# Performance work log

Hardware: AMD Instinct MI355X
Metric: run time of the kernel (lower is better)

Reference implementation:

```python
import jax, jax.numpy as jnp
import numpy as np


def setup_inputs() -> dict:
    key = jax.random.key(0)
    ks = jax.random.split(key, 5)
    n, raw, d, h = 1024, 128, 128, 256
    s = lambda fan: 1.0 / np.sqrt(fan)
    return {
        "x": jax.random.normal(ks[0], (n, raw), jnp.float32),
        "W_enc": jax.random.normal(ks[1], (raw, d), jnp.float32) * s(raw),
        "b_enc": jnp.zeros((d,), jnp.float32),
        "W1": jax.random.normal(ks[2], (2 * d, h), jnp.float32) * s(2 * d),
        "b1": jnp.zeros((h,), jnp.float32),
        "W2": jax.random.normal(ks[3], (h, 1), jnp.float32) * s(h),
        "b2": jnp.zeros((1,), jnp.float32),
    }


def reference(x, W_enc, b_enc, W1, b1, W2, b2):
    # pathVAE.encode stand-in: linear projection to latent mean
    z = x @ W_enc + b_enc                      # [n, d]
    n, d = z.shape
    # Original builds feat[i, j] = concat(z[j], z[i]) of shape [n*n, 2d],
    # then Linear(2d->h). Split W1 so the quadratic concat is never built:
    # h[i, j] = z[j] @ W1[:d] + z[i] @ W1[d:] + b1
    A = z @ W1[:d]                             # acts on the "a" (j) half
    B = z @ W1[d:]                             # acts on the "b" (i) half
    hmat = A[None, :, :] + B[:, None, :] + b1  # [n, n, h]
    hmat = jax.nn.selu(hmat)
    o = hmat @ W2 + b2                         # [n, n, 1]
    o = jax.nn.hard_sigmoid(o)                 # relu6(x+3)/6, same as torch
    return o.reshape(n, n)
```

## Files before the change

kernel.cpp:

```cpp
#include <hip/hip_runtime.h>
#include <math.h>


#define LOG2E       1.4426950408889634f
#define SELU_AS     1.7580993408473766f
#define S_OVER_L2E  0.7282921587620419f

typedef float v2f __attribute__((ext_vector_type(2)));
typedef _Float16 v2h __attribute__((ext_vector_type(2)));
typedef unsigned int u32;

__global__ __launch_bounds__(256) void prep_kernel(
    const float* __restrict__ x, const float* __restrict__ W_enc,
    const float* __restrict__ b_enc, const float* __restrict__ W1,
    const float* __restrict__ b1, const float* __restrict__ W2,
    const float* __restrict__ b2, u32* __restrict__ PAa,
    u32* __restrict__ PAe, u32* __restrict__ PBb, u32* __restrict__ PBe,
    u32* __restrict__ W2h, float* __restrict__ basep)
{
    __shared__ float zs[512];
    int t = threadIdx.x, b = blockIdx.x;
    if (b < 256) {
        int r0 = b << 2;
        int r = t >> 6;
        int dd = (t & 63) << 1;
        const float* xr = x + (size_t)(r0 + r) * 128;
        v2f z = { b_enc[dd], b_enc[dd + 1] };
#pragma unroll 8
        for (int dl = 0; dl < 128; ++dl) {
            float xv = xr[dl];
            v2f xx = { xv, xv };
            v2f wv = *(const v2f*)(W_enc + (size_t)dl * 128 + dd);
            z = __builtin_elementwise_fma(xx, wv, z);
        }
        zs[r * 128 + dd] = z.x;
        zs[r * 128 + dd + 1] = z.y;
        __syncthreads();

        int c = t;
        float b1c = b1[c];
        float accA0 = 0.f, accA1 = 0.f, accA2 = 0.f, accA3 = 0.f;
        float accB0 = b1c, accB1 = b1c, accB2 = b1c, accB3 = b1c;
        const float* w1a = W1 + c;
        const float* w1b = W1 + 128 * 256 + c;
#pragma unroll 4
        for (int dl = 0; dl < 128; ++dl) {
            float wa = w1a[(size_t)dl * 256];
            float wb = w1b[(size_t)dl * 256];
            float z0 = zs[dl], z1 = zs[128 + dl], z2 = zs[256 + dl], z3 = zs[384 + dl];
            accA0 = fmaf(z0, wa, accA0); accB0 = fmaf(z0, wb, accB0);
            accA1 = fmaf(z1, wa, accA1); accB1 = fmaf(z1, wb, accB1);
            accA2 = fmaf(z2, wa, accA2); accB2 = fmaf(z2, wb, accB2);
            accA3 = fmaf(z3, wa, accA3); accB3 = fmaf(z3, wb, accB3);
        }
        float ar[4] = { accA0 * LOG2E, accA1 * LOG2E, accA2 * LOG2E, accA3 * LOG2E };
        float br[4] = { accB0 * LOG2E, accB1 * LOG2E, accB2 * LOG2E, accB3 * LOG2E };
        u32 pa[4], pe[4], pb[4], pf[4];
        bool odd = (c & 1);
#pragma unroll
        for (int r2 = 0; r2 < 4; ++r2) {
            float er = __builtin_amdgcn_exp2f(ar[r2]);
            float fr = __builtin_amdgcn_exp2f(br[r2]);
            float aN = __shfl_xor(ar[r2], 1);
            float eN = __shfl_xor(er, 1);
            float bN = __shfl_xor(br[r2], 1);
            float fN = __shfl_xor(fr, 1);
            pa[r2] = __builtin_bit_cast(u32, __builtin_amdgcn_cvt_pkrtz(ar[r2], aN));
            pe[r2] = __builtin_bit_cast(u32, __builtin_amdgcn_cvt_pkrtz(er, eN));
            pb[r2] = __builtin_bit_cast(u32, __builtin_amdgcn_cvt_pkrtz(bN, br[r2]));
            pf[r2] = __builtin_bit_cast(u32, __builtin_amdgcn_cvt_pkrtz(fN, fr));
        }
        size_t o = (size_t)(c >> 1) * 1024 + r0;
        if (!odd) {
            *(uint4*)(PAa + o) = make_uint4(pa[0], pa[1], pa[2], pa[3]);
            *(uint4*)(PAe + o) = make_uint4(pe[0], pe[1], pe[2], pe[3]);
        } else {
            *(uint4*)(PBb + o) = make_uint4(pb[0], pb[1], pb[2], pb[3]);
            *(uint4*)(PBe + o) = make_uint4(pf[0], pf[1], pf[2], pf[3]);
        }
    } else {
        if (t < 128) {
            W2h[t] = __builtin_bit_cast(u32,
                __builtin_amdgcn_cvt_pkrtz(W2[2 * t], W2[2 * t + 1]));
        }
        if (t < 64) {
            float s = W2[t] + W2[t + 64] + W2[t + 128] + W2[t + 192];
#pragma unroll
            for (int o = 32; o > 0; o >>= 1) s += __shfl_down(s, o);
            if (t == 0) basep[0] = fmaf(-SELU_AS, s, b2[0]);
        }
    }
}

__global__ __launch_bounds__(256) void pair_kernel(
    const u32* __restrict__ PAa, const u32* __restrict__ PAe,
    const u32* __restrict__ PBb, const u32* __restrict__ PBe,
    const u32* __restrict__ W2h, const float* __restrict__ basep,
    float* __restrict__ out)
{
    __shared__ __align__(16) u32 Aa[64 * 64];
    __shared__ __align__(16) u32 Ae[64 * 64];
    __shared__ __align__(16) u32 Bb[64 * 64];
    __shared__ __align__(16) u32 Be[64 * 64];

    int t = threadIdx.x;
    int bj64 = blockIdx.x << 6, bi64 = blockIdx.y << 6;
    int tjx = t & 15, tiy = t >> 4;
    int tj4 = tjx << 2, ti4 = tiy << 2;

    float acc1[4][4], acc2[4][4];
#pragma unroll
    for (int i = 0; i < 4; ++i)
#pragma unroll
        for (int j = 0; j < 4; ++j) { acc1[i][j] = 0.f; acc2[i][j] = 0.f; }

    const v2h hzero = { (_Float16)0.f, (_Float16)0.f };
    const v2h hone  = { (_Float16)1.f, (_Float16)1.f };

    for (int ch = 0; ch < 2; ++ch) {
        if (ch) __syncthreads();
#pragma unroll
        for (int p = 0; p < 4; ++p) {
            int q = (p << 8) + t;
            int k2l = q >> 4;
            int jq = (q & 15) << 2;
            size_t go = (size_t)((ch << 6) + k2l) * 1024;
            *(uint4*)&Aa[q << 2] = *(const uint4*)(PAa + go + bj64 + jq);
            *(uint4*)&Ae[q << 2] = *(const uint4*)(PAe + go + bj64 + jq);
            *(uint4*)&Bb[q << 2] = *(const uint4*)(PBb + go + bi64 + jq);
            *(uint4*)&Be[q << 2] = *(const uint4*)(PBe + go + bi64 + jq);
        }
        __syncthreads();

        const u32* W2c = W2h + (ch << 6);
#pragma unroll 4
        for (int k2 = 0; k2 < 64; ++k2) {
            v2h w2 = __builtin_bit_cast(v2h, W2c[k2]);
            uint4 qa = *(const uint4*)&Aa[(k2 << 6) + tj4];
            uint4 qe = *(const uint4*)&Ae[(k2 << 6) + tj4];
            uint4 qb = *(const uint4*)&Bb[(k2 << 6) + ti4];
            uint4 qf = *(const uint4*)&Be[(k2 << 6) + ti4];
            v2h a[4] = { __builtin_bit_cast(v2h, qa.x), __builtin_bit_cast(v2h, qa.y),
                         __builtin_bit_cast(v2h, qa.z), __builtin_bit_cast(v2h, qa.w) };
            v2h e[4] = { __builtin_bit_cast(v2h, qe.x), __builtin_bit_cast(v2h, qe.y),
                         __builtin_bit_cast(v2h, qe.z), __builtin_bit_cast(v2h, qe.w) };
            v2h bb[4] = { __builtin_bit_cast(v2h, qb.x), __builtin_bit_cast(v2h, qb.y),
                          __builtin_bit_cast(v2h, qb.z), __builtin_bit_cast(v2h, qb.w) };
            v2h ff[4] = { __builtin_bit_cast(v2h, qf.x), __builtin_bit_cast(v2h, qf.y),
                          __builtin_bit_cast(v2h, qf.z), __builtin_bit_cast(v2h, qf.w) };
#pragma unroll
            for (int i = 0; i < 4; ++i) {
#pragma unroll
                for (int j = 0; j < 4; ++j) {
                    v2h t2 = a[j] + bb[i];
                    v2h p2 = e[j] * ff[i];
                    v2h m2 = __builtin_elementwise_max(t2, hzero);
                    v2h n2 = __builtin_elementwise_min(p2, hone);
                    acc1[i][j] = __builtin_amdgcn_fdot2(m2, w2, acc1[i][j], false);
                    acc2[i][j] = __builtin_amdgcn_fdot2(n2, w2, acc2[i][j], false);
                }
            }
        }
    }

    float base = basep[0];
#pragma unroll
    for (int i = 0; i < 4; ++i) {
        float4 o;
        float v0 = fmaf(S_OVER_L2E, acc1[i][0], fmaf(SELU_AS, acc2[i][0], base));
        float v1 = fmaf(S_OVER_L2E, acc1[i][1], fmaf(SELU_AS, acc2[i][1], base));
        float v2 = fmaf(S_OVER_L2E, acc1[i][2], fmaf(SELU_AS, acc2[i][2], base));
        float v3 = fmaf(S_OVER_L2E, acc1[i][3], fmaf(SELU_AS, acc2[i][3], base));
        o.x = __saturatef(v0 * (1.0f / 6.0f) + 0.5f);
        o.y = __saturatef(v1 * (1.0f / 6.0f) + 0.5f);
        o.z = __saturatef(v2 * (1.0f / 6.0f) + 0.5f);
        o.w = __saturatef(v3 * (1.0f / 6.0f) + 0.5f);
        *(float4*)(out + (size_t)(bi64 + ti4 + i) * 1024 + bj64 + tj4) = o;
    }
}

extern "C" void kernel_launch(void* const* d_in, const int* in_sizes, int n_in,
                              void* d_out, int out_size, void* d_ws, size_t ws_size,
                              hipStream_t stream) {
    const float* x     = (const float*)d_in[0];
    const float* W_enc = (const float*)d_in[1];
    const float* b_enc = (const float*)d_in[2];
    const float* W1    = (const float*)d_in[3];
    const float* b1    = (const float*)d_in[4];
    const float* W2    = (const float*)d_in[5];
    const float* b2    = (const float*)d_in[6];
    float* out = (float*)d_out;

    u32* ws = (u32*)d_ws;
    const int PLANE = 128 * 1024;
    u32* PAa = ws;
    u32* PAe = ws + PLANE;
    u32* PBb = ws + 2 * PLANE;
    u32* PBe = ws + 3 * PLANE;
    u32* W2h = ws + 4 * PLANE;
    float* basep = (float*)(ws + 4 * PLANE + 128);

    prep_kernel<<<257, 256, 0, stream>>>(x, W_enc, b_enc, W1, b1, W2, b2,
                                         PAa, PAe, PBb, PBe, W2h, basep);
    pair_kernel<<<dim3(16, 16), 256, 0, stream>>>(PAa, PAe, PBb, PBe, W2h,
                                                  basep, out);
}
```

Before: 116.5 us.

## Split pair kernel over hidden dimension and reduce partials in combine kernel

```diff
diff --git a/kernel.cpp b/kernel.cpp
--- a/kernel.cpp
+++ b/kernel.cpp
@@ -16,7 +16,7 @@
     const float* __restrict__ b1, const float* __restrict__ W2,
     const float* __restrict__ b2, u32* __restrict__ PAa,
     u32* __restrict__ PAe, u32* __restrict__ PBb, u32* __restrict__ PBe,
-    u32* __restrict__ W2h, float* __restrict__ basep)
+    u32* __restrict__ W2m, u32* __restrict__ W2e, float* __restrict__ basep)
 {
     __shared__ float zs[512];
     int t = threadIdx.x, b = blockIdx.x;
@@ -80,8 +80,11 @@
         }
     } else {
         if (t < 128) {
-            W2h[t] = __builtin_bit_cast(u32,
-                __builtin_amdgcn_cvt_pkrtz(W2[2 * t], W2[2 * t + 1]));
+            float w0 = W2[2 * t], w1 = W2[2 * t + 1];
+            W2m[t] = __builtin_bit_cast(u32,
+                __builtin_amdgcn_cvt_pkrtz(S_OVER_L2E * w0, S_OVER_L2E * w1));
+            W2e[t] = __builtin_bit_cast(u32,
+                __builtin_amdgcn_cvt_pkrtz(SELU_AS * w0, SELU_AS * w1));
         }
         if (t < 64) {
             float s = W2[t] + W2[t + 64] + W2[t + 128] + W2[t + 192];
@@ -92,91 +95,101 @@
     }
 }
 
-__global__ __launch_bounds__(256) void pair_kernel(
+__global__ __launch_bounds__(256, 4) void pair_kernel(
     const u32* __restrict__ PAa, const u32* __restrict__ PAe,
     const u32* __restrict__ PBb, const u32* __restrict__ PBe,
-    const u32* __restrict__ W2h, const float* __restrict__ basep,
+    const u32* __restrict__ W2m, const u32* __restrict__ W2e,
+    float* __restrict__ P)
+{
+    __shared__ __align__(16) u32 Aa[32 * 64];
+    __shared__ __align__(16) u32 Ae[32 * 64];
+    __shared__ __align__(16) u32 Bb[32 * 64];
+    __shared__ __align__(16) u32 Be[32 * 64];
+
+    int t = threadIdx.x;
+    int bj64 = blockIdx.x << 6, bi64 = blockIdx.y << 6;
+    int kc = blockIdx.z;
+    int tj4 = (t & 15) << 2, ti4 = (t >> 4) << 2;
+
+    float acc[4][4];
+#pragma unroll
+    for (int i = 0; i < 4; ++i)
+#pragma unroll
+        for (int j = 0; j < 4; ++j) acc[i][j] = 0.f;
+
+    const v2h hzero = { (_Float16)0.f, (_Float16)0.f };
+    const v2h hone  = { (_Float16)1.f, (_Float16)1.f };
+
+#pragma unroll
+    for (int p = 0; p < 2; ++p) {
+        int q = (p << 8) + t;
+        int k2l = q >> 4;
+        int jq = (q & 15) << 2;
+        size_t go = (size_t)((kc << 5) + k2l) * 1024;
+        *(uint4*)&Aa[q << 2] = *(const uint4*)(PAa + go + bj64 + jq);
+        *(uint4*)&Ae[q << 2] = *(const uint4*)(PAe + go + bj64 + jq);
+        *(uint4*)&Bb[q << 2] = *(const uint4*)(PBb + go + bi64 + jq);
+        *(uint4*)&Be[q << 2] = *(const uint4*)(PBe + go + bi64 + jq);
+    }
+    __syncthreads();
+
+    const u32* Wm = W2m + (kc << 5);
+    const u32* We = W2e + (kc << 5);
+#pragma unroll 4
+    for (int k2 = 0; k2 < 32; ++k2) {
+        v2h w2m = __builtin_bit_cast(v2h, Wm[k2]);
+        v2h w2e = __builtin_bit_cast(v2h, We[k2]);
+        uint4 qa = *(const uint4*)&Aa[(k2 << 6) + tj4];
+        uint4 qe = *(const uint4*)&Ae[(k2 << 6) + tj4];
+        uint4 qb = *(const uint4*)&Bb[(k2 << 6) + ti4];
+        uint4 qf = *(const uint4*)&Be[(k2 << 6) + ti4];
+        v2h a[4] = { __builtin_bit_cast(v2h, qa.x), __builtin_bit_cast(v2h, qa.y),
+                     __builtin_bit_cast(v2h, qa.z), __builtin_bit_cast(v2h, qa.w) };
+        v2h e[4] = { __builtin_bit_cast(v2h, qe.x), __builtin_bit_cast(v2h, qe.y),
+                     __builtin_bit_cast(v2h, qe.z), __builtin_bit_cast(v2h, qe.w) };
+        v2h bb[4] = { __builtin_bit_cast(v2h, qb.x), __builtin_bit_cast(v2h, qb.y),
+                      __builtin_bit_cast(v2h, qb.z), __builtin_bit_cast(v2h, qb.w) };
+        v2h ff[4] = { __builtin_bit_cast(v2h, qf.x), __builtin_bit_cast(v2h, qf.y),
+                      __builtin_bit_cast(v2h, qf.z), __builtin_bit_cast(v2h, qf.w) };
+#pragma unroll
+        for (int i = 0; i < 4; ++i) {
+#pragma unroll
+            for (int j = 0; j < 4; ++j) {
+                v2h t2 = a[j] + bb[i];
+                v2h p2 = e[j] * ff[i];
+                v2h m2 = __builtin_elementwise_max(t2, hzero);
+                v2h n2 = __builtin_elementwise_min(p2, hone);
+                acc[i][j] = __builtin_amdgcn_fdot2(m2, w2m, acc[i][j], false);
+                acc[i][j] = __builtin_amdgcn_fdot2(n2, w2e, acc[i][j], false);
+            }
+        }
+    }
+
+    float* Pc = P + ((size_t)kc << 20);
+#pragma unroll
+    for (int i = 0; i < 4; ++i) {
+        float4 o;
+        o.x = acc[i][0]; o.y = acc[i][1]; o.z = acc[i][2]; o.w = acc[i][3];
+        *(float4*)(Pc + (size_t)(bi64 + ti4 + i) * 1024 + bj64 + tj4) = o;
+    }
+}
+
+__global__ __launch_bounds__(256) void combine_kernel(
+    const float* __restrict__ P, const float* __restrict__ basep,
     float* __restrict__ out)
 {
-    __shared__ __align__(16) u32 Aa[64 * 64];
-    __shared__ __align__(16) u32 Ae[64 * 64];
-    __shared__ __align__(16) u32 Bb[64 * 64];
-    __shared__ __align__(16) u32 Be[64 * 64];
-
-    int t = threadIdx.x;
-    int bj64 = blockIdx.x << 6, bi64 = blockIdx.y << 6;
-    int tjx = t & 15, tiy = t >> 4;
-    int tj4 = tjx << 2, ti4 = tiy << 2;
-
-    float acc1[4][4], acc2[4][4];
-#pragma unroll
-    for (int i = 0; i < 4; ++i)
-#pragma unroll
-        for (int j = 0; j < 4; ++j) { acc1[i][j] = 0.f; acc2[i][j] = 0.f; }
-
-    const v2h hzero = { (_Float16)0.f, (_Float16)0.f };
-    const v2h hone  = { (_Float16)1.f, (_Float16)1.f };
-
-    for (int ch = 0; ch < 2; ++ch) {
-        if (ch) __syncthreads();
-#pragma unroll
-        for (int p = 0; p < 4; ++p) {
-            int q = (p << 8) + t;
-            int k2l = q >> 4;
-            int jq = (q & 15) << 2;
-            size_t go = (size_t)((ch << 6) + k2l) * 1024;
-            *(uint4*)&Aa[q << 2] = *(const uint4*)(PAa + go + bj64 + jq);
-            *(uint4*)&Ae[q << 2] = *(const uint4*)(PAe + go + bj64 + jq);
-            *(uint4*)&Bb[q << 2] = *(const uint4*)(PBb + go + bi64 + jq);
-            *(uint4*)&Be[q << 2] = *(const uint4*)(PBe + go + bi64 + jq);
-        }
-        __syncthreads();
-
-        const u32* W2c = W2h + (ch << 6);
-#pragma unroll 4
-        for (int k2 = 0; k2 < 64; ++k2) {
-            v2h w2 = __builtin_bit_cast(v2h, W2c[k2]);
-            uint4 qa = *(const uint4*)&Aa[(k2 << 6) + tj4];
-            uint4 qe = *(const uint4*)&Ae[(k2 << 6) + tj4];
-            uint4 qb = *(const uint4*)&Bb[(k2 << 6) + ti4];
-            uint4 qf = *(const uint4*)&Be[(k2 << 6) + ti4];
-            v2h a[4] = { __builtin_bit_cast(v2h, qa.x), __builtin_bit_cast(v2h, qa.y),
-                         __builtin_bit_cast(v2h, qa.z), __builtin_bit_cast(v2h, qa.w) };
-            v2h e[4] = { __builtin_bit_cast(v2h, qe.x), __builtin_bit_cast(v2h, qe.y),
-                         __builtin_bit_cast(v2h, qe.z), __builtin_bit_cast(v2h, qe.w) };
-            v2h bb[4] = { __builtin_bit_cast(v2h, qb.x), __builtin_bit_cast(v2h, qb.y),
-                          __builtin_bit_cast(v2h, qb.z), __builtin_bit_cast(v2h, qb.w) };
-            v2h ff[4] = { __builtin_bit_cast(v2h, qf.x), __builtin_bit_cast(v2h, qf.y),
-                          __builtin_bit_cast(v2h, qf.z), __builtin_bit_cast(v2h, qf.w) };
-#pragma unroll
-            for (int i = 0; i < 4; ++i) {
-#pragma unroll
-                for (int j = 0; j < 4; ++j) {
-                    v2h t2 = a[j] + bb[i];
-                    v2h p2 = e[j] * ff[i];
-                    v2h m2 = __builtin_elementwise_max(t2, hzero);
-                    v2h n2 = __builtin_elementwise_min(p2, hone);
-                    acc1[i][j] = __builtin_amdgcn_fdot2(m2, w2, acc1[i][j], false);
-                    acc2[i][j] = __builtin_amdgcn_fdot2(n2, w2, acc2[i][j], false);
-                }
-            }
-        }
-    }
-
+    int idx = (blockIdx.x * 256 + threadIdx.x) << 2;
+    float4 p0 = *(const float4*)(P + idx);
+    float4 p1 = *(const float4*)(P + (1 << 20) + idx);
+    float4 p2 = *(const float4*)(P + (2 << 20) + idx);
+    float4 p3 = *(const float4*)(P + (3 << 20) + idx);
     float base = basep[0];
-#pragma unroll
-    for (int i = 0; i < 4; ++i) {
-        float4 o;
-        float v0 = fmaf(S_OVER_L2E, acc1[i][0], fmaf(SELU_AS, acc2[i][0], base));
-        float v1 = fmaf(S_OVER_L2E, acc1[i][1], fmaf(SELU_AS, acc2[i][1], base));
-        float v2 = fmaf(S_OVER_L2E, acc1[i][2], fmaf(SELU_AS, acc2[i][2], base));
-        float v3 = fmaf(S_OVER_L2E, acc1[i][3], fmaf(SELU_AS, acc2[i][3], base));
-        o.x = __saturatef(v0 * (1.0f / 6.0f) + 0.5f);
-        o.y = __saturatef(v1 * (1.0f / 6.0f) + 0.5f);
-        o.z = __saturatef(v2 * (1.0f / 6.0f) + 0.5f);
-        o.w = __saturatef(v3 * (1.0f / 6.0f) + 0.5f);
-        *(float4*)(out + (size_t)(bi64 + ti4 + i) * 1024 + bj64 + tj4) = o;
-    }
+    float4 o;
+    o.x = __saturatef((p0.x + p1.x + p2.x + p3.x + base) * (1.0f / 6.0f) + 0.5f);
+    o.y = __saturatef((p0.y + p1.y + p2.y + p3.y + base) * (1.0f / 6.0f) + 0.5f);
+    o.z = __saturatef((p0.z + p1.z + p2.z + p3.z + base) * (1.0f / 6.0f) + 0.5f);
+    o.w = __saturatef((p0.w + p1.w + p2.w + p3.w + base) * (1.0f / 6.0f) + 0.5f);
+    *(float4*)(out + idx) = o;
 }
 
 extern "C" void kernel_launch(void* const* d_in, const int* in_sizes, int n_in,
@@ -197,11 +210,14 @@
     u32* PAe = ws + PLANE;
     u32* PBb = ws + 2 * PLANE;
     u32* PBe = ws + 3 * PLANE;
-    u32* W2h = ws + 4 * PLANE;
-    float* basep = (float*)(ws + 4 * PLANE + 128);
+    u32* W2m = ws + 4 * PLANE;
+    u32* W2e = ws + 4 * PLANE + 128;
+    float* basep = (float*)(ws + 4 * PLANE + 256);
+    float* P = (float*)(ws + 4 * PLANE + 512);
 
     prep_kernel<<<257, 256, 0, stream>>>(x, W_enc, b_enc, W1, b1, W2, b2,
-                                         PAa, PAe, PBb, PBe, W2h, basep);
-    pair_kernel<<<dim3(16, 16), 256, 0, stream>>>(PAa, PAe, PBb, PBe, W2h,
-                                                  basep, out);
-}
+                                         PAa, PAe, PBb, PBe, W2m, W2e, basep);
+    pair_kernel<<<dim3(16, 16, 4), 256, 0, stream>>>(PAa, PAe, PBb, PBe,
+                                                     W2m, W2e, P);
+    combine_kernel<<<1024, 256, 0, stream>>>(P, basep, out);
+}
```

After: 117.5 us. About the same (+0.8%).
